# Kernel optimization log

Measured on AMD Instinct MI355X. Metric: run time of the kernel, lower is better.

## Reference

```python
import jax, jax.numpy as jnp
import numpy as np

EPS = 1e-5  # nn.BatchNorm1d default eps


def setup_inputs() -> dict:
    key = jax.random.key(0)
    ks = jax.random.split(key, 8)
    N_NODES, N_EDGES = 50000, 800000
    D_NODE, D_EDGE, HID, NCLS = 128, 64, 256, 8
    D_IN = D_EDGE + 2 * D_NODE  # 320
    return {
        "n_feats": jax.random.normal(ks[0], (N_NODES, D_NODE), dtype=jnp.float32),
        "edge_feats": jax.random.normal(ks[1], (N_EDGES, D_EDGE), dtype=jnp.float32),
        "src_idx": jax.random.randint(ks[2], (N_EDGES,), 0, N_NODES, dtype=jnp.int64),
        "dst_idx": jax.random.randint(ks[3], (N_EDGES,), 0, N_NODES, dtype=jnp.int64),
        "W1": jax.random.normal(ks[4], (HID, D_IN), dtype=jnp.float32) * (1.0 / np.sqrt(D_IN)),
        "b1": jnp.zeros((HID,), dtype=jnp.float32),
        "gamma": jnp.ones((HID,), dtype=jnp.float32),
        "beta": jnp.zeros((HID,), dtype=jnp.float32),
        "W2": jax.random.normal(ks[5], (NCLS, HID), dtype=jnp.float32) * (1.0 / np.sqrt(HID)),
        "b2": jnp.zeros((NCLS,), dtype=jnp.float32),
    }


def reference(n_feats, edge_feats, src_idx, dst_idx, W1, b1, gamma, beta, W2, b2):
    # gather-concat: [E, d_edge + 2*d_node]
    h = jnp.concatenate([edge_feats, n_feats[src_idx], n_feats[dst_idx]], axis=1)
    # Linear 1
    z = jnp.einsum("ei,hi->eh", h, W1) + b1
    # BatchNorm1d in training mode: batch mean / biased variance over edges
    mu = jnp.mean(z, axis=0)
    var = jnp.mean(jnp.square(z - mu), axis=0)
    zn = (z - mu) * jax.lax.rsqrt(var + EPS) * gamma + beta
    # Linear 2 + LogSoftmax(dim=1)
    logits = jnp.einsum("eh,ch->ec", zn, W2) + b2
    return jax.nn.log_softmax(logits, axis=1)
```

## Files before the change

### kernel.cpp

```cpp
#include <hip/hip_runtime.h>
#include <hip/hip_bf16.h>


#define N_EDGES 800000
#define N_NODES 50000

typedef __attribute__((ext_vector_type(8))) short short8;
typedef __attribute__((ext_vector_type(4))) float f32x4;

#define WS_SUM   0
#define WS_SQ    16384
#define WS_CVEC  32768
#define WS_FLAG  32832
#define WS_MBIG  33280
#define WS_MB    43520
#define WS_MF    45568
#define WS_W1B   55808
#define WS_PS    262144
#define WS_PD    2097152
#define WS_NFB   4194304
#define WS_FAST_NEED (4u << 20)
#define WS_BIG_NEED  16994304u

__device__ __forceinline__ ushort f2bf(float f) {
    union { float f; unsigned int u; } x; x.f = f;
    unsigned int r = x.u + 0x7FFFu + ((x.u >> 16) & 1u);
    return (ushort)(r >> 16);
}
__device__ __forceinline__ short8 cvt8(const float* __restrict__ p) {
    short8 r;
    #pragma unroll
    for (int i = 0; i < 8; i++) r[i] = (short)f2bf(p[i]);
    return r;
}
__device__ __forceinline__ short8 cvtpair(uint4 a, uint4 b) {
    unsigned int v[8] = {a.x, a.y, a.z, a.w, b.x, b.y, b.z, b.w};
    short8 r;
    #pragma unroll
    for (int i = 0; i < 8; i++) {
        unsigned int u = v[i];
        unsigned int rr = u + 0x7FFFu + ((u >> 16) & 1u);
        r[i] = (short)(rr >> 16);
    }
    return r;
}

__global__ void detect_kernel(const int* __restrict__ src,
                              const int* __restrict__ dst, int* flag) {
    int t = threadIdx.x;
    int v = src[2 * t + 1] | dst[2 * t + 1];
    #pragma unroll
    for (int o = 32; o >= 1; o >>= 1) v |= __shfl_xor(v, o);
    if (t == 0) *flag = (v == 0) ? 1 : 0;
}

__global__ __launch_bounds__(256) void prep_kernel(const float* __restrict__ W1,
                                                   ushort* __restrict__ W1b) {
    const int i = (blockIdx.x * 256 + threadIdx.x) * 4;
    const float4 v = *(const float4*)(W1 + i);
    ushort4 o;
    o.x = f2bf(v.x); o.y = f2bf(v.y); o.z = f2bf(v.z); o.w = f2bf(v.w);
    *(ushort4*)(W1b + i) = o;
}

__global__ __launch_bounds__(256) void prep_nf_kernel(const float* __restrict__ nf,
                                                      ushort* __restrict__ nfb) {
    const long i = ((long)blockIdx.x * 256 + threadIdx.x) * 4;
    const float4 v = *(const float4*)(nf + i);
    ushort4 o;
    o.x = f2bf(v.x); o.y = f2bf(v.y); o.z = f2bf(v.z); o.w = f2bf(v.w);
    *(ushort4*)(nfb + i) = o;
}

template <bool NFB>
__global__ __launch_bounds__(256) void gemm1_stats_kernel(
    const float* __restrict__ nf, const ushort* __restrict__ nfb,
    const float* __restrict__ ef,
    const int* __restrict__ src, const int* __restrict__ dst,
    const ushort* __restrict__ W1b, const int* __restrict__ flag,
    float* __restrict__ g_sum, float* __restrict__ g_sq)
{
    __shared__ ushort a_lds[10][64 * 40];
    __shared__ float s_sum[256];
    __shared__ float s_sq[256];

    const int t    = threadIdx.x;
    const int lane = t & 63;
    const int wave = t >> 6;
    const int quad = lane >> 4;
    const int l15  = lane & 15;

    s_sum[t] = 0.f; s_sq[t] = 0.f;

    const int wide = *flag;
    const int r = t >> 2, chunk = t & 3;
    const long e  = (long)blockIdx.x * 64 + r;
    const int si = src[e << wide], di = dst[e << wide];
    const float* pe = ef + e * 64 + chunk * 8;

    uint4 pe0[2], pe1[2];
    pe0[0] = *(const uint4*)pe;        pe0[1] = *(const uint4*)(pe + 4);
    pe1[0] = *(const uint4*)(pe + 32); pe1[1] = *(const uint4*)(pe + 36);

    if constexpr (NFB) {
        const ushort* psb = nfb + (long)si * 128 + chunk * 8;
        const ushort* pdb = nfb + (long)di * 128 + chunk * 8;
        short8 g[8];
        #pragma unroll
        for (int i = 0; i < 4; i++) g[i]     = *(const short8*)(psb + i * 32);
        #pragma unroll
        for (int i = 0; i < 4; i++) g[4 + i] = *(const short8*)(pdb + i * 32);
        *(short8*)&a_lds[0][r * 40 + chunk * 8] = cvtpair(pe0[0], pe0[1]);
        *(short8*)&a_lds[1][r * 40 + chunk * 8] = cvtpair(pe1[0], pe1[1]);
        #pragma unroll
        for (int i = 0; i < 8; i++)
            *(short8*)&a_lds[2 + i][r * 40 + chunk * 8] = g[i];
    } else {
        const float* ps = nf + (long)si * 128 + chunk * 8;
        const float* pd = nf + (long)di * 128 + chunk * 8;
        uint4 pn[16];
        #pragma unroll
        for (int i = 0; i < 4; i++) {
            pn[i * 2]     = *(const uint4*)(ps + i * 32);
            pn[i * 2 + 1] = *(const uint4*)(ps + i * 32 + 4);
        }
        #pragma unroll
        for (int i = 0; i < 4; i++) {
            pn[8 + i * 2]     = *(const uint4*)(pd + i * 32);
            pn[8 + i * 2 + 1] = *(const uint4*)(pd + i * 32 + 4);
        }
        *(short8*)&a_lds[0][r * 40 + chunk * 8] = cvtpair(pe0[0], pe0[1]);
        *(short8*)&a_lds[1][r * 40 + chunk * 8] = cvtpair(pe1[0], pe1[1]);
        #pragma unroll
        for (int i = 0; i < 8; i++)
            *(short8*)&a_lds[2 + i][r * 40 + chunk * 8] =
                cvtpair(pn[i * 2], pn[i * 2 + 1]);
    }
    __syncthreads();

    f32x4 acc[4][4];
    #pragma unroll
    for (int a = 0; a < 4; a++)
        #pragma unroll
        for (int b = 0; b < 4; b++) acc[a][b] = (f32x4){0.f, 0.f, 0.f, 0.f};

    const ushort* wbase = W1b + (wave * 64 + l15) * 320 + quad * 8;

    #pragma unroll
    for (int ks = 0; ks < 10; ks++) {
        short8 bfr[4];
        #pragma unroll
        for (int in = 0; in < 4; in++)
            bfr[in] = *(const short8*)(wbase + in * 16 * 320 + ks * 32);
        short8 afr[4];
        #pragma unroll
        for (int mb = 0; mb < 4; mb++)
            afr[mb] = *(const short8*)
                &a_lds[ks][(mb * 16 + l15) * 40 + quad * 8];
        __builtin_amdgcn_s_setprio(1);
        #pragma unroll
        for (int mb = 0; mb < 4; mb++)
            #pragma unroll
            for (int in = 0; in < 4; in++)
                acc[mb][in] = __builtin_amdgcn_mfma_f32_16x16x32_bf16(
                    afr[mb], bfr[in], acc[mb][in], 0, 0, 0);
        __builtin_amdgcn_s_setprio(0);
    }

    #pragma unroll
    for (int in = 0; in < 4; in++) {
        const int col = wave * 64 + in * 16 + l15;
        float s = 0.f, q = 0.f;
        #pragma unroll
        for (int mb = 0; mb < 4; mb++)
            #pragma unroll
            for (int j = 0; j < 4; j++) {
                float v = acc[mb][in][j];
                s += v; q += v * v;
            }
        s += __shfl_xor(s, 16); s += __shfl_xor(s, 32);
        q += __shfl_xor(q, 16); q += __shfl_xor(q, 32);
        if (quad == 0) { atomicAdd(&s_sum[col], s); atomicAdd(&s_sq[col], q); }
    }
    __syncthreads();
    const int slot = blockIdx.x & 15;
    atomicAdd(&g_sum[slot * 256 + t], s_sum[t]);
    atomicAdd(&g_sq[slot * 256 + t], s_sq[t]);
}

__global__ __launch_bounds__(256) void fold_kernel(
    const float* __restrict__ gamma, const float* __restrict__ beta,
    const float* __restrict__ W1, const float* __restrict__ b1,
    const float* __restrict__ W2, const float* __restrict__ b2,
    const float* __restrict__ g_sum, const float* __restrict__ g_sq,
    ushort* __restrict__ Mbig, ushort* __restrict__ Mb,
    float* __restrict__ Mf, float* __restrict__ Cvec)
{
    __shared__ float a_sh[256][8];
    __shared__ float red[8];
    __shared__ float mk_sh[64][8];
    const int t = threadIdx.x;

    float ssum = 0.f, ssq = 0.f;
    #pragma unroll
    for (int s = 0; s < 16; s++) {
        ssum += g_sum[s * 256 + t];
        ssq  += g_sq[s * 256 + t];
    }
    const float invE   = 1.0f / (float)N_EDGES;
    const float mu_acc = ssum * invE;
    float var = ssq * invE - mu_acc * mu_acc;
    var = fmaxf(var, 0.f);
    const float b1v = b1[t];
    const float mu  = mu_acc + b1v;
    const float g   = gamma[t] * rsqrtf(var + 1e-5f);
    const float sh  = b1v * g + beta[t] - mu * g;

    if (t < 8) red[t] = 0.f;
    ((float*)mk_sh)[t] = 0.f;
    ((float*)mk_sh)[t + 256] = 0.f;
    __syncthreads();
    #pragma unroll
    for (int c = 0; c < 8; c++) {
        const float w = W2[c * 256 + t];
        a_sh[t][c] = w * g;
        if (blockIdx.x == 0) atomicAdd(&red[c], w * sh);
    }
    __syncthreads();

    const int k  = blockIdx.x * 64 + (t & 63);
    const int q4 = t >> 6;
    float m[8] = {0.f, 0.f, 0.f, 0.f, 0.f, 0.f, 0.f, 0.f};
    for (int hh = q4 * 64; hh < q4 * 64 + 64; hh++) {
        const float w1 = W1[hh * 320 + k];
        #pragma unroll
        for (int c = 0; c < 8; c++) m[c] += a_sh[hh][c] * w1;
    }
    #pragma unroll
    for (int c = 0; c < 8; c++) atomicAdd(&mk_sh[t & 63][c], m[c]);
    __syncthreads();

    if (t < 64) {
        const int kk = blockIdx.x * 64 + t;
        #pragma unroll
        for (int c = 0; c < 8; c++) {
            const float mv = mk_sh[t][c];
            Mf[c * 320 + kk]   = mv;
            Mbig[c * 320 + kk] = f2bf(mv);
            if (kk < 64) Mb[c * 64 + kk] = f2bf(mv);
        }
        #pragma unroll
        for (int c = 8; c < 16; c++) {
            Mbig[c * 320 + kk] = 0;
            if (kk < 64) Mb[c * 64 + kk] = 0;
        }
    }
    if (blockIdx.x == 0) {
        if (t < 8)       Cvec[t] = b2[t] + red[t];
        else if (t < 16) Cvec[t] = 0.f;
    }
}

__global__ __launch_bounds__(256) void nodeproj_kernel(
    const float* __restrict__ nf, const float* __restrict__ Mf,
    float* __restrict__ Ps, float* __restrict__ Pd)
{
    __shared__ float Ms[8][128];
    __shared__ float Md[8][128];
    const int t = threadIdx.x;
    #pragma unroll
    for (int i = 0; i < 4; i++) {
        const int f = t + i * 256;
        Ms[f >> 7][f & 127] = Mf[(f >> 7) * 320 + 64  + (f & 127)];
        Md[f >> 7][f & 127] = Mf[(f >> 7) * 320 + 192 + (f & 127)];
    }
    __syncthreads();
    const int n = blockIdx.x * 256 + t;
    if (n >= N_NODES) return;
    float as[8] = {0,0,0,0,0,0,0,0}, ad[8] = {0,0,0,0,0,0,0,0};
    for (int k = 0; k < 128; k += 4) {
        const float4 v = *(const float4*)(nf + (long)n * 128 + k);
        #pragma unroll
        for (int c = 0; c < 8; c++) {
            const float4 ms = *(const float4*)&Ms[c][k];
            const float4 md = *(const float4*)&Md[c][k];
            as[c] += v.x * ms.x + v.y * ms.y + v.z * ms.z + v.w * ms.w;
            ad[c] += v.x * md.x + v.y * md.y + v.z * md.z + v.w * md.w;
        }
    }
    #pragma unroll
    for (int c = 0; c < 8; c++) {
        Ps[n * 8 + c] = as[c];
        Pd[n * 8 + c] = ad[c];
    }
}

__global__ __launch_bounds__(256) void edge_out_kernel(
    const float* __restrict__ ef, const int* __restrict__ src,
    const int* __restrict__ dst, const int* __restrict__ flag,
    const ushort* __restrict__ Mb, const float* __restrict__ Ps,
    const float* __restrict__ Pd, const float* __restrict__ Cvec,
    float* __restrict__ out)
{
    __shared__ float pv_sh[4][64][9];
    const int t    = threadIdx.x;
    const int lane = t & 63;
    const int wave = t >> 6;
    const int quad = lane >> 4;
    const int l15  = lane & 15;
    const int wide = *flag;
    const long eb  = (long)blockIdx.x * 256 + wave * 64;

    const long ei = (eb + lane) << wide;
    const int sidx = src[ei], didx = dst[ei];
    const float4 s0 = *(const float4*)(Ps + sidx * 8);
    const float4 s1 = *(const float4*)(Ps + sidx * 8 + 4);
    const float4 d0 = *(const float4*)(Pd + didx * 8);
    const float4 d1 = *(const float4*)(Pd + didx * 8 + 4);

    uint4 ea[4][2], eb4[4][2];
    #pragma unroll
    for (int mb = 0; mb < 4; mb++)
        #pragma unroll
        for (int ks = 0; ks < 2; ks++) {
            const float* p = ef + (eb + mb * 16 + l15) * 64 + ks * 32 + quad * 8;
            ea[mb][ks]  = *(const uint4*)p;
            eb4[mb][ks] = *(const uint4*)(p + 4);
        }

    pv_sh[wave][lane][0] = s0.x + d0.x;
    pv_sh[wave][lane][1] = s0.y + d0.y;
    pv_sh[wave][lane][2] = s0.z + d0.z;
    pv_sh[wave][lane][3] = s0.w + d0.w;
    pv_sh[wave][lane][4] = s1.x + d1.x;
    pv_sh[wave][lane][5] = s1.y + d1.y;
    pv_sh[wave][lane][6] = s1.z + d1.z;
    pv_sh[wave][lane][7] = s1.w + d1.w;

    f32x4 acc[4];
    #pragma unroll
    for (int mb = 0; mb < 4; mb++) acc[mb] = (f32x4){0.f, 0.f, 0.f, 0.f};

    const ushort* bbase = Mb + l15 * 64 + quad * 8;
    #pragma unroll
    for (int ks = 0; ks < 2; ks++) {
        short8 bfr = *(const short8*)(bbase + ks * 32);
        #pragma unroll
        for (int mb = 0; mb < 4; mb++)
            acc[mb] = __builtin_amdgcn_mfma_f32_16x16x32_bf16(
                cvtpair(ea[mb][ks], eb4[mb][ks]), bfr, acc[mb], 0, 0, 0);
    }
    __syncthreads();

    const float bv = Cvec[l15];
    #pragma unroll
    for (int mb = 0; mb < 4; mb++) {
        #pragma unroll
        for (int j = 0; j < 4; j++) {
            const int er = mb * 16 + quad * 4 + j;
            const float pv = (l15 < 8) ? pv_sh[wave][er][l15] : 0.f;
            float x = acc[mb][j] + bv + pv;
            float m = x;
            m = fmaxf(m, __shfl_xor(m, 1));
            m = fmaxf(m, __shfl_xor(m, 2));
            m = fmaxf(m, __shfl_xor(m, 4));
            float sx = __expf(x - m);
            sx += __shfl_xor(sx, 1);
            sx += __shfl_xor(sx, 2);
            sx += __shfl_xor(sx, 4);
            const float o = x - m - __logf(sx);
            if (l15 < 8) out[(eb + er) * 8 + l15] = o;
        }
    }
}

__global__ __launch_bounds__(256) void out_kernel(
    const float* __restrict__ nf, const float* __restrict__ ef,
    const int* __restrict__ src, const int* __restrict__ dst,
    const int* __restrict__ flag, const ushort* __restrict__ M,
    const float* __restrict__ Cvec, float* __restrict__ out)
{
    const int t    = threadIdx.x;
    const int lane = t & 63;
    const int wave = t >> 6;
    const int quad = lane >> 4;
    const int l15  = lane & 15;
    const int wide = *flag;
    const long eb  = (long)blockIdx.x * 256 + wave * 64;

    const float* pe[4]; const float* ps[4]; const float* pd[4];
    #pragma unroll
    for (int mb = 0; mb < 4; mb++) {
        const long e  = eb + mb * 16 + l15;
        const int si = src[e << wide], di = dst[e << wide];
        pe[mb] = ef + e * 64;
        ps[mb] = nf + (long)si * 128;
        pd[mb] = nf + (long)di * 128;
    }
    f32x4 acc[4];
    #pragma unroll
    for (int mb = 0; mb < 4; mb++) acc[mb] = (f32x4){0.f, 0.f, 0.f, 0.f};
    const ushort* bbase = M + l15 * 320 + quad * 8;
    #pragma unroll
    for (int ks = 0; ks < 10; ks++) {
        const int k0 = ks * 32;
        short8 bfr = *(const short8*)(bbase + k0);
        const int koff = k0 + quad * 8;
        #pragma unroll
        for (int mb = 0; mb < 4; mb++) {
            const float* p = (ks < 2) ? (pe[mb] + koff)
                           : (ks < 6) ? (ps[mb] + (koff - 64))
                                      : (pd[mb] + (koff - 192));
            acc[mb] = __builtin_amdgcn_mfma_f32_16x16x32_bf16(
                cvt8(p), bfr, acc[mb], 0, 0, 0);
        }
    }
    const float bv = Cvec[l15];
    #pragma unroll
    for (int mb = 0; mb < 4; mb++)
        #pragma unroll
        for (int j = 0; j < 4; j++) {
            float x = acc[mb][j] + bv;
            float m = x;
            m = fmaxf(m, __shfl_xor(m, 1));
            m = fmaxf(m, __shfl_xor(m, 2));
            m = fmaxf(m, __shfl_xor(m, 4));
            float sx = __expf(x - m);
            sx += __shfl_xor(sx, 1);
            sx += __shfl_xor(sx, 2);
            sx += __shfl_xor(sx, 4);
            const float o = x - m - __logf(sx);
            if (l15 < 8)
                out[(eb + mb * 16 + quad * 4 + j) * 8 + l15] = o;
        }
}

extern "C" void kernel_launch(void* const* d_in, const int* in_sizes, int n_in,
                              void* d_out, int out_size, void* d_ws, size_t ws_size,
                              hipStream_t stream) {
    const float* nf    = (const float*)d_in[0];
    const float* ef    = (const float*)d_in[1];
    const int*   src   = (const int*)d_in[2];
    const int*   dst   = (const int*)d_in[3];
    const float* W1    = (const float*)d_in[4];
    const float* b1    = (const float*)d_in[5];
    const float* gamma = (const float*)d_in[6];
    const float* beta  = (const float*)d_in[7];
    const float* W2    = (const float*)d_in[8];
    const float* b2    = (const float*)d_in[9];

    char*   ws    = (char*)d_ws;
    float*  g_sum = (float*)(ws + WS_SUM);
    float*  g_sq  = (float*)(ws + WS_SQ);
    float*  Cvec  = (float*)(ws + WS_CVEC);
    int*    flag  = (int*)(ws + WS_FLAG);
    ushort* Mbig  = (ushort*)(ws + WS_MBIG);
    ushort* Mb    = (ushort*)(ws + WS_MB);
    float*  Mf    = (float*)(ws + WS_MF);
    ushort* W1b   = (ushort*)(ws + WS_W1B);
    float*  Ps    = (float*)(ws + WS_PS);
    float*  Pd    = (float*)(ws + WS_PD);
    ushort* nfb   = (ushort*)(ws + WS_NFB);
    float*  out   = (float*)d_out;

    const bool fast = ws_size >= (size_t)WS_FAST_NEED;
    const bool big  = ws_size >= (size_t)WS_BIG_NEED;

    hipMemsetAsync(ws, 0, 33280, stream);
    detect_kernel<<<1, 64, 0, stream>>>(src, dst, flag);
    prep_kernel<<<80, 256, 0, stream>>>(W1, W1b);
    if (big) {
        prep_nf_kernel<<<6250, 256, 0, stream>>>(nf, nfb);
        gemm1_stats_kernel<true><<<N_EDGES / 64, 256, 0, stream>>>(
            nf, nfb, ef, src, dst, W1b, flag, g_sum, g_sq);
    } else {
        gemm1_stats_kernel<false><<<N_EDGES / 64, 256, 0, stream>>>(
            nf, nfb, ef, src, dst, W1b, flag, g_sum, g_sq);
    }
    fold_kernel<<<5, 256, 0, stream>>>(gamma, beta, W1, b1, W2, b2,
                                       g_sum, g_sq, Mbig, Mb, Mf, Cvec);
    if (fast) {
        nodeproj_kernel<<<(N_NODES + 255) / 256, 256, 0, stream>>>(nf, Mf, Ps, Pd);
        edge_out_kernel<<<N_EDGES / 256, 256, 0, stream>>>(ef, src, dst, flag,
                                                           Mb, Ps, Pd, Cvec, out);
    } else {
        out_kernel<<<N_EDGES / 256, 256, 0, stream>>>(nf, ef, src, dst, flag,
                                                      Mbig, Cvec, out);
    }
}
```

Before: 645.2 us.

## Fuse prep and fold/nodeproj kernels, swizzle LDS, prefetch GEMM operands

```diff
diff --git a/kernel.cpp b/kernel.cpp
--- a/kernel.cpp
+++ b/kernel.cpp
@@ -45,6 +45,10 @@
     return r;
 }
 
+__device__ __forceinline__ int aidx(int s, int r, int c) {
+    return ((s * 64 + r) * 4 + (c ^ ((r >> 1) & 3))) * 8;
+}
+
 __global__ void detect_kernel(const int* __restrict__ src,
                               const int* __restrict__ dst, int* flag) {
     int t = threadIdx.x;
@@ -63,13 +67,40 @@
     *(ushort4*)(W1b + i) = o;
 }
 
-__global__ __launch_bounds__(256) void prep_nf_kernel(const float* __restrict__ nf,
-                                                      ushort* __restrict__ nfb) {
-    const long i = ((long)blockIdx.x * 256 + threadIdx.x) * 4;
-    const float4 v = *(const float4*)(nf + i);
-    ushort4 o;
-    o.x = f2bf(v.x); o.y = f2bf(v.y); o.z = f2bf(v.z); o.w = f2bf(v.w);
-    *(ushort4*)(nfb + i) = o;
+__global__ __launch_bounds__(256) void prep_all_kernel(
+    const float* __restrict__ nf, const float* __restrict__ W1,
+    const int* __restrict__ src, const int* __restrict__ dst,
+    ushort* __restrict__ nfb, ushort* __restrict__ W1b,
+    float* __restrict__ zreg, int* __restrict__ flag)
+{
+    const int t = threadIdx.x;
+    const int b = blockIdx.x;
+    if (b < 3125) {
+        const long i = (long)b * 2048 + t * 8;
+        const float4 v0 = *(const float4*)(nf + i);
+        const float4 v1 = *(const float4*)(nf + i + 4);
+        short8 o;
+        o[0] = (short)f2bf(v0.x); o[1] = (short)f2bf(v0.y);
+        o[2] = (short)f2bf(v0.z); o[3] = (short)f2bf(v0.w);
+        o[4] = (short)f2bf(v1.x); o[5] = (short)f2bf(v1.y);
+        o[6] = (short)f2bf(v1.z); o[7] = (short)f2bf(v1.w);
+        *(short8*)(nfb + i) = o;
+    } else if (b < 3205) {
+        const int i = (b - 3125) * 1024 + t * 4;
+        const float4 v = *(const float4*)(W1 + i);
+        ushort4 o;
+        o.x = f2bf(v.x); o.y = f2bf(v.y); o.z = f2bf(v.z); o.w = f2bf(v.w);
+        *(ushort4*)(W1b + i) = o;
+    } else {
+        for (int i = t; i < 8320; i += 256) zreg[i] = 0.f;
+        __syncthreads();
+        if (t < 64) {
+            int v = src[2 * t + 1] | dst[2 * t + 1];
+            #pragma unroll
+            for (int o = 32; o >= 1; o >>= 1) v |= __shfl_xor(v, o);
+            if (t == 0) *flag = (v == 0) ? 1 : 0;
+        }
+    }
 }
 
 template <bool NFB>
@@ -80,9 +111,7 @@
     const ushort* __restrict__ W1b, const int* __restrict__ flag,
     float* __restrict__ g_sum, float* __restrict__ g_sq)
 {
-    __shared__ ushort a_lds[10][64 * 40];
-    __shared__ float s_sum[256];
-    __shared__ float s_sq[256];
+    __shared__ ushort a_lds[10 * 64 * 32];
 
     const int t    = threadIdx.x;
     const int lane = t & 63;
@@ -90,8 +119,6 @@
     const int quad = lane >> 4;
     const int l15  = lane & 15;
 
-    s_sum[t] = 0.f; s_sq[t] = 0.f;
-
     const int wide = *flag;
     const int r = t >> 2, chunk = t & 3;
     const long e  = (long)blockIdx.x * 64 + r;
@@ -102,6 +129,15 @@
     pe0[0] = *(const uint4*)pe;        pe0[1] = *(const uint4*)(pe + 4);
     pe1[0] = *(const uint4*)(pe + 32); pe1[1] = *(const uint4*)(pe + 36);
 
+    const ushort* wbase = W1b + (wave * 64 + l15) * 320 + quad * 8;
+    short8 bpre[2][4];
+    #pragma unroll
+    for (int in = 0; in < 4; in++)
+        bpre[0][in] = *(const short8*)(wbase + in * 16 * 320);
+    #pragma unroll
+    for (int in = 0; in < 4; in++)
+        bpre[1][in] = *(const short8*)(wbase + in * 16 * 320 + 32);
+
     if constexpr (NFB) {
         const ushort* psb = nfb + (long)si * 128 + chunk * 8;
         const ushort* pdb = nfb + (long)di * 128 + chunk * 8;
@@ -110,11 +146,11 @@
         for (int i = 0; i < 4; i++) g[i]     = *(const short8*)(psb + i * 32);
         #pragma unroll
         for (int i = 0; i < 4; i++) g[4 + i] = *(const short8*)(pdb + i * 32);
-        *(short8*)&a_lds[0][r * 40 + chunk * 8] = cvtpair(pe0[0], pe0[1]);
-        *(short8*)&a_lds[1][r * 40 + chunk * 8] = cvtpair(pe1[0], pe1[1]);
+        *(short8*)&a_lds[aidx(0, r, chunk)] = cvtpair(pe0[0], pe0[1]);
+        *(short8*)&a_lds[aidx(1, r, chunk)] = cvtpair(pe1[0], pe1[1]);
         #pragma unroll
         for (int i = 0; i < 8; i++)
-            *(short8*)&a_lds[2 + i][r * 40 + chunk * 8] = g[i];
+            *(short8*)&a_lds[aidx(2 + i, r, chunk)] = g[i];
     } else {
         const float* ps = nf + (long)si * 128 + chunk * 8;
         const float* pd = nf + (long)di * 128 + chunk * 8;
@@ -129,11 +165,11 @@
             pn[8 + i * 2]     = *(const uint4*)(pd + i * 32);
             pn[8 + i * 2 + 1] = *(const uint4*)(pd + i * 32 + 4);
         }
-        *(short8*)&a_lds[0][r * 40 + chunk * 8] = cvtpair(pe0[0], pe0[1]);
-        *(short8*)&a_lds[1][r * 40 + chunk * 8] = cvtpair(pe1[0], pe1[1]);
+        *(short8*)&a_lds[aidx(0, r, chunk)] = cvtpair(pe0[0], pe0[1]);
+        *(short8*)&a_lds[aidx(1, r, chunk)] = cvtpair(pe1[0], pe1[1]);
         #pragma unroll
         for (int i = 0; i < 8; i++)
-            *(short8*)&a_lds[2 + i][r * 40 + chunk * 8] =
+            *(short8*)&a_lds[aidx(2 + i, r, chunk)] =
                 cvtpair(pn[i * 2], pn[i * 2 + 1]);
     }
     __syncthreads();
@@ -144,29 +180,41 @@
         #pragma unroll
         for (int b = 0; b < 4; b++) acc[a][b] = (f32x4){0.f, 0.f, 0.f, 0.f};
 
-    const ushort* wbase = W1b + (wave * 64 + l15) * 320 + quad * 8;
+    short8 acur[4], anext[4];
+    #pragma unroll
+    for (int mb = 0; mb < 4; mb++)
+        acur[mb] = *(const short8*)&a_lds[aidx(0, mb * 16 + l15, quad)];
 
     #pragma unroll
     for (int ks = 0; ks < 10; ks++) {
-        short8 bfr[4];
-        #pragma unroll
-        for (int in = 0; in < 4; in++)
-            bfr[in] = *(const short8*)(wbase + in * 16 * 320 + ks * 32);
-        short8 afr[4];
-        #pragma unroll
-        for (int mb = 0; mb < 4; mb++)
-            afr[mb] = *(const short8*)
-                &a_lds[ks][(mb * 16 + l15) * 40 + quad * 8];
+        short8 bcur[4];
+        #pragma unroll
+        for (int in = 0; in < 4; in++) bcur[in] = bpre[ks & 1][in];
+        if (ks < 8) {
+            #pragma unroll
+            for (int in = 0; in < 4; in++)
+                bpre[ks & 1][in] =
+                    *(const short8*)(wbase + in * 16 * 320 + (ks + 2) * 32);
+        }
+        if (ks < 9) {
+            #pragma unroll
+            for (int mb = 0; mb < 4; mb++)
+                anext[mb] = *(const short8*)
+                    &a_lds[aidx(ks + 1, mb * 16 + l15, quad)];
+        }
         __builtin_amdgcn_s_setprio(1);
         #pragma unroll
         for (int mb = 0; mb < 4; mb++)
             #pragma unroll
             for (int in = 0; in < 4; in++)
                 acc[mb][in] = __builtin_amdgcn_mfma_f32_16x16x32_bf16(
-                    afr[mb], bfr[in], acc[mb][in], 0, 0, 0);
+                    acur[mb], bcur[in], acc[mb][in], 0, 0, 0);
         __builtin_amdgcn_s_setprio(0);
-    }
-
+        #pragma unroll
+        for (int mb = 0; mb < 4; mb++) acur[mb] = anext[mb];
+    }
+
+    const int slot = blockIdx.x & 15;
     #pragma unroll
     for (int in = 0; in < 4; in++) {
         const int col = wave * 64 + in * 16 + l15;
@@ -180,12 +228,11 @@
             }
         s += __shfl_xor(s, 16); s += __shfl_xor(s, 32);
         q += __shfl_xor(q, 16); q += __shfl_xor(q, 32);
-        if (quad == 0) { atomicAdd(&s_sum[col], s); atomicAdd(&s_sq[col], q); }
-    }
-    __syncthreads();
-    const int slot = blockIdx.x & 15;
-    atomicAdd(&g_sum[slot * 256 + t], s_sum[t]);
-    atomicAdd(&g_sq[slot * 256 + t], s_sq[t]);
+        if (quad == 0) {
+            atomicAdd(&g_sum[slot * 256 + col], s);
+            atomicAdd(&g_sq[slot * 256 + col], q);
+        }
+    }
 }
 
 __global__ __launch_bounds__(256) void fold_kernel(
@@ -258,6 +305,94 @@
     if (blockIdx.x == 0) {
         if (t < 8)       Cvec[t] = b2[t] + red[t];
         else if (t < 16) Cvec[t] = 0.f;
+    }
+}
+
+__global__ __launch_bounds__(256) void fold_nodeproj_kernel(
+    const float* __restrict__ gamma, const float* __restrict__ beta,
+    const float* __restrict__ W1, const float* __restrict__ b1,
+    const float* __restrict__ W2, const float* __restrict__ b2,
+    const float* __restrict__ g_sum, const float* __restrict__ g_sq,
+    const float* __restrict__ nf, ushort* __restrict__ Mb,
+    float* __restrict__ Cvec, float* __restrict__ Ps, float* __restrict__ Pd)
+{
+    __shared__ float a_sh[256][8];
+    __shared__ float red[8];
+    __shared__ float Ms[8][128];
+    __shared__ float Md[8][128];
+    const int t = threadIdx.x;
+
+    float ssum = 0.f, ssq = 0.f;
+    #pragma unroll
+    for (int s = 0; s < 16; s++) {
+        ssum += g_sum[s * 256 + t];
+        ssq  += g_sq[s * 256 + t];
+    }
+    const float invE   = 1.0f / (float)N_EDGES;
+    const float mu_acc = ssum * invE;
+    float var = ssq * invE - mu_acc * mu_acc;
+    var = fmaxf(var, 0.f);
+    const float b1v = b1[t];
+    const float mu  = mu_acc + b1v;
+    const float g   = gamma[t] * rsqrtf(var + 1e-5f);
+    const float sh  = b1v * g + beta[t] - mu * g;
+
+    if (t < 8) red[t] = 0.f;
+    __syncthreads();
+    #pragma unroll
+    for (int c = 0; c < 8; c++) {
+        const float w = W2[c * 256 + t];
+        a_sh[t][c] = w * g;
+        if (blockIdx.x == 0) atomicAdd(&red[c], w * sh);
+    }
+    __syncthreads();
+
+    float m[8] = {0.f, 0.f, 0.f, 0.f, 0.f, 0.f, 0.f, 0.f};
+    for (int hh = 0; hh < 256; hh++) {
+        const float w1 = W1[hh * 320 + 64 + t];
+        #pragma unroll
+        for (int c = 0; c < 8; c++) m[c] += a_sh[hh][c] * w1;
+    }
+    #pragma unroll
+    for (int c = 0; c < 8; c++) {
+        if (t < 128) Ms[c][t] = m[c];
+        else         Md[c][t - 128] = m[c];
+    }
+    if (blockIdx.x == 0) {
+        if (t < 64) {
+            float mm[8] = {0.f, 0.f, 0.f, 0.f, 0.f, 0.f, 0.f, 0.f};
+            for (int hh = 0; hh < 256; hh++) {
+                const float w1 = W1[hh * 320 + t];
+                #pragma unroll
+                for (int c = 0; c < 8; c++) mm[c] += a_sh[hh][c] * w1;
+            }
+            #pragma unroll
+            for (int c = 0; c < 8; c++)  Mb[c * 64 + t] = f2bf(mm[c]);
+            #pragma unroll
+            for (int c = 8; c < 16; c++) Mb[c * 64 + t] = 0;
+        }
+        if (t < 8)       Cvec[t] = b2[t] + red[t];
+        else if (t < 16) Cvec[t] = 0.f;
+    }
+    __syncthreads();
+
+    const int n = blockIdx.x * 256 + t;
+    if (n >= N_NODES) return;
+    float as[8] = {0,0,0,0,0,0,0,0}, ad[8] = {0,0,0,0,0,0,0,0};
+    for (int k = 0; k < 128; k += 4) {
+        const float4 v = *(const float4*)(nf + (long)n * 128 + k);
+        #pragma unroll
+        for (int c = 0; c < 8; c++) {
+            const float4 ms = *(const float4*)&Ms[c][k];
+            const float4 md = *(const float4*)&Md[c][k];
+            as[c] += v.x * ms.x + v.y * ms.y + v.z * ms.z + v.w * ms.w;
+            ad[c] += v.x * md.x + v.y * md.y + v.z * md.z + v.w * md.w;
+        }
+    }
+    #pragma unroll
+    for (int c = 0; c < 8; c++) {
+        Ps[n * 8 + c] = as[c];
+        Pd[n * 8 + c] = ad[c];
     }
 }
 
@@ -350,7 +485,6 @@
             acc[mb] = __builtin_amdgcn_mfma_f32_16x16x32_bf16(
                 cvtpair(ea[mb][ks], eb4[mb][ks]), bfr, acc[mb], 0, 0, 0);
     }
-    __syncthreads();
 
     const float bv = Cvec[l15];
     #pragma unroll
@@ -466,25 +600,30 @@
     const bool fast = ws_size >= (size_t)WS_FAST_NEED;
     const bool big  = ws_size >= (size_t)WS_BIG_NEED;
 
-    hipMemsetAsync(ws, 0, 33280, stream);
-    detect_kernel<<<1, 64, 0, stream>>>(src, dst, flag);
-    prep_kernel<<<80, 256, 0, stream>>>(W1, W1b);
     if (big) {
-        prep_nf_kernel<<<6250, 256, 0, stream>>>(nf, nfb);
+        prep_all_kernel<<<3206, 256, 0, stream>>>(nf, W1, src, dst, nfb, W1b,
+                                                  (float*)ws, flag);
         gemm1_stats_kernel<true><<<N_EDGES / 64, 256, 0, stream>>>(
             nf, nfb, ef, src, dst, W1b, flag, g_sum, g_sq);
-    } else {
-        gemm1_stats_kernel<false><<<N_EDGES / 64, 256, 0, stream>>>(
-            nf, nfb, ef, src, dst, W1b, flag, g_sum, g_sq);
-    }
-    fold_kernel<<<5, 256, 0, stream>>>(gamma, beta, W1, b1, W2, b2,
-                                       g_sum, g_sq, Mbig, Mb, Mf, Cvec);
-    if (fast) {
-        nodeproj_kernel<<<(N_NODES + 255) / 256, 256, 0, stream>>>(nf, Mf, Ps, Pd);
+        fold_nodeproj_kernel<<<(N_NODES + 255) / 256, 256, 0, stream>>>(
+            gamma, beta, W1, b1, W2, b2, g_sum, g_sq, nf, Mb, Cvec, Ps, Pd);
         edge_out_kernel<<<N_EDGES / 256, 256, 0, stream>>>(ef, src, dst, flag,
                                                            Mb, Ps, Pd, Cvec, out);
     } else {
-        out_kernel<<<N_EDGES / 256, 256, 0, stream>>>(nf, ef, src, dst, flag,
-                                                      Mbig, Cvec, out);
-    }
-}
+        hipMemsetAsync(ws, 0, 33280, stream);
+        detect_kernel<<<1, 64, 0, stream>>>(src, dst, flag);
+        prep_kernel<<<80, 256, 0, stream>>>(W1, W1b);
+        gemm1_stats_kernel<false><<<N_EDGES / 64, 256, 0, stream>>>(
+            nf, nfb, ef, src, dst, W1b, flag, g_sum, g_sq);
+        fold_kernel<<<5, 256, 0, stream>>>(gamma, beta, W1, b1, W2, b2,
+                                           g_sum, g_sq, Mbig, Mb, Mf, Cvec);
+        if (fast) {
+            nodeproj_kernel<<<(N_NODES + 255) / 256, 256, 0, stream>>>(nf, Mf, Ps, Pd);
+            edge_out_kernel<<<N_EDGES / 256, 256, 0, stream>>>(ef, src, dst, flag,
+                                                               Mb, Ps, Pd, Cvec, out);
+        } else {
+            out_kernel<<<N_EDGES / 256, 256, 0, stream>>>(nf, ef, src, dst, flag,
+                                                          Mbig, Cvec, out);
+        }
+    }
+}
```

Result: faster. 623.1 us (-3.4%).
